# Optimization experiments

Measured on AMD Instinct MI355X. Metric: run time of the kernel, lower is better.

The kernel has to match this reference:

```python
import jax, jax.numpy as jnp
import numpy as np
from jax import lax

B, L = 8192, 64
N_VALUES, EMBED, HIDDEN, OUT = 1000, 64, 128, 128


def setup_inputs() -> dict:
    key = jax.random.key(0)
    ks = jax.random.split(key, 8)
    s = 0.1  # weight scale ~ 1/sqrt(hidden)
    return {
        "x": jax.random.randint(ks[0], (B, L), 0, N_VALUES),
        "embed": jax.random.normal(ks[1], (N_VALUES, EMBED), jnp.float32) * s,
        "W_ih": jax.random.normal(ks[2], (3 * HIDDEN, EMBED), jnp.float32) * s,
        "W_hh": jax.random.normal(ks[3], (3 * HIDDEN, HIDDEN), jnp.float32) * s,
        "b_ih": jax.random.normal(ks[4], (3 * HIDDEN,), jnp.float32) * s,
        "b_hh": jax.random.normal(ks[5], (3 * HIDDEN,), jnp.float32) * s,
        "W_out": jax.random.normal(ks[6], (OUT, HIDDEN), jnp.float32) * s,
        "b_out": jax.random.normal(ks[7], (OUT,), jnp.float32) * s,
    }


def _gru_encode(x, embed, W_ih, W_hh, b_ih, b_hh, W_out, b_out):
    e = embed[x]  # [B, L, E] embedding lookup
    H = W_hh.shape[1]
    # Precompute input-to-gate projections for all timesteps (batched GEMM).
    xg = jnp.einsum('ble,ge->blg', e, W_ih) + b_ih  # [B, L, 3H]

    def step(h, xg_t):
        hg = h @ W_hh.T + b_hh  # [B, 3H]
        xr, xz, xn = jnp.split(xg_t, 3, axis=-1)
        hr, hz, hn = jnp.split(hg, 3, axis=-1)
        r = jax.nn.sigmoid(xr + hr)
        z = jax.nn.sigmoid(xz + hz)
        n = jnp.tanh(xn + r * hn)  # PyTorch GRU: r gates the hidden 'new' term
        h_new = (1.0 - z) * n + z * h
        return h_new, None

    h0 = jnp.zeros((x.shape[0], H), e.dtype)
    h_last, _ = lax.scan(step, h0, jnp.swapaxes(xg, 0, 1))  # scan over time
    return h_last @ W_out.T + b_out  # [B, OUT]


def reference(x, embed, W_ih, W_hh, b_ih, b_hh, W_out, b_out):
    return _gru_encode(x, embed, W_ih, W_hh, b_ih, b_hh, W_out, b_out)
```

## Files before the change

kernel.cpp:

```cpp
#include <hip/hip_runtime.h>


typedef __bf16 bf16x8 __attribute__((ext_vector_type(8)));
typedef float  f32x4  __attribute__((ext_vector_type(4)));
typedef int    int4v  __attribute__((ext_vector_type(4)));
typedef unsigned int uint2v __attribute__((ext_vector_type(2)));

#define NV   1000
#define EMB  64
#define HD   128
#define G3   384
#define SEQ  64
#define BB   16

#define SC_RZ (-1.4426950408889634f)
#define SC_N  ( 2.8853900817779268f)

__device__ __forceinline__ float bflo(unsigned int word) {
    return __builtin_bit_cast(float, word << 16);
}
__device__ __forceinline__ float bfhi(unsigned int word) {
    return __builtin_bit_cast(float, word & 0xffff0000u);
}

__global__ void g_table_kernel(const float* __restrict__ embed,
                               const float* __restrict__ W_ih,
                               const float* __restrict__ b_ih,
                               const float* __restrict__ b_hh,
                               unsigned short* __restrict__ Gpk)
{
    __shared__ float emb[EMB];
    const int v = blockIdx.x;
    const int g = threadIdx.x;
    if (g < EMB) emb[g] = embed[v * EMB + g];
    __syncthreads();
    const float* wr = W_ih + g * EMB;
    float s = b_ih[g] + (g < 2 * HD ? b_hh[g] : 0.f);
    #pragma unroll
    for (int e = 0; e < EMB; e += 4) {
        const float4 w4 = *(const float4*)(wr + e);
        s += w4.x * emb[e] + w4.y * emb[e + 1] + w4.z * emb[e + 2] + w4.w * emb[e + 3];
    }
    const int hid = g & 127, gate = g >> 7;
    s *= (gate < 2) ? SC_RZ : SC_N;
    const int w8 = hid >> 4, c16i = hid & 15;
    Gpk[((v * 8 + w8) * 16 + c16i) * 4 + gate] =
        __builtin_bit_cast(unsigned short, (__bf16)s);
}

#define GRU_STEP(P, T)                                                             \
  {                                                                                \
    __builtin_amdgcn_s_setprio(1);                                                 \
    int4v tk = {0, 0, 0, 0};                                                       \
    if ((T) < SEQ - 1) tk = *(const int4v*)&xl[((T) + 1) * BB + quad * 4];         \
    f32x4 acc[3];                                                                  \
    float xn_[4];                                                                  \
    _Pragma("unroll") for (int j = 0; j < 4; ++j) {                                \
      acc[0][j] = bflo(pf[j][0]);                                \
      acc[1][j] = bfhi(pf[j][0]);                                \
      acc[2][j] = bnw;                                           \
      xn_[j]    = bflo(pf[j][1]);                                \
    }                                                                              \
    _Pragma("unroll") for (int ks = 0; ks < 4; ++ks) {                             \
      const bf16x8 af = *(const bf16x8*)(hbase + (P) * 4096 + aoff[ks]);           \
      _Pragma("unroll") for (int gate = 0; gate < 3; ++gate)                       \
        acc[gate] = __builtin_amdgcn_mfma_f32_16x16x32_bf16(                       \
            af, wf[gate][ks], acc[gate], 0, 0, 0);                                 \
    }                                                                              \
    if ((T) < SEQ - 1) {                                                           \
      _Pragma("unroll") for (int j = 0; j < 4; ++j)                                \
        pf[j] = *(const uint2v*)(gbase + (unsigned)(tk[j] * 1024 + goff));         \
    }                                                                              \
    __builtin_amdgcn_s_setprio(0);                                                 \
    _Pragma("unroll") for (int j = 0; j < 4; ++j) {                                \
      const float Er = __builtin_amdgcn_exp2f(acc[0][j]);                          \
      const float r  = __builtin_amdgcn_rcpf(1.f + Er);                            \
      const float Ez = __builtin_amdgcn_exp2f(acc[1][j]);                          \
      const float a1 = 1.f + Ez;                                                   \
      const float v  = __builtin_fmaf(r, acc[2][j], xn_[j]);                       \
      const float En = __builtin_amdgcn_exp2f(v);                                  \
      const float a2 = 1.f + En;                                                   \
      const float m  = En - 1.f;                                                   \
      const float num = __builtin_fmaf(hreg[j], a2, Ez * m);                       \
      const float rd  = __builtin_amdgcn_rcpf(a1 * a2);                            \
      const float hn  = num * rd;                                                  \
      hreg[j] = hn;                                                                \
      *(unsigned short*)(hbase + (1 - (P)) * 4096 + woff[j]) =                     \
          __builtin_bit_cast(unsigned short, (__bf16)hn);                          \
    }                                                                              \
    asm volatile("s_waitcnt lgkmcnt(0)" ::: "memory");                             \
    __builtin_amdgcn_s_barrier();                                                  \
    __builtin_amdgcn_sched_barrier(0);                                             \
  }

__global__ __launch_bounds__(512, 4) void gru_kernel(
    const int*   __restrict__ x,    const unsigned short* __restrict__ Gpk,
    const float* __restrict__ Whh,  const float* __restrict__ bhh,
    const float* __restrict__ Wout, const float* __restrict__ bout,
    float* __restrict__ out)
{
    __shared__ unsigned short hA[2 * BB * HD];
    __shared__ int xl[SEQ * BB];

    const int tid  = threadIdx.x;
    const int lane = tid & 63;
    const int w    = tid >> 6;
    const int c16  = lane & 15;
    const int quad = lane >> 4;
    const int br0  = blockIdx.x * BB;

    #pragma unroll
    for (int i = 0; i < 2; ++i) {
        const int idx = i * 512 + tid;
        const int r = idx >> 6;
        const int t = idx & 63;
        xl[t * BB + r] = x[(br0 + r) * SEQ + t];
    }
    {
        unsigned int* hA32 = (unsigned int*)hA;
        #pragma unroll
        for (int i = 0; i < 2; ++i)
            hA32[i * 512 + tid] = 0u;
    }

    bf16x8 wf[3][4];
    #pragma unroll
    for (int gate = 0; gate < 3; ++gate)
    #pragma unroll
    for (int ks = 0; ks < 4; ++ks) {
        const float sc = (gate < 2) ? SC_RZ : SC_N;
        const int col = gate * HD + w * 16 + c16;
        const float* p = Whh + col * HD + ks * 32 + quad * 4;
        const float4 a = *(const float4*)p;
        const float4 b = *(const float4*)(p + 16);
        bf16x8 f;
        f[0] = (__bf16)(sc * a.x); f[1] = (__bf16)(sc * a.y);
        f[2] = (__bf16)(sc * a.z); f[3] = (__bf16)(sc * a.w);
        f[4] = (__bf16)(sc * b.x); f[5] = (__bf16)(sc * b.y);
        f[6] = (__bf16)(sc * b.z); f[7] = (__bf16)(sc * b.w);
        wf[gate][ks] = f;
    }

    const float bnw = SC_N * bhh[2 * HD + w * 16 + c16];

    int aoff[4];
    #pragma unroll
    for (int ks = 0; ks < 4; ++ks)
        aoff[ks] = c16 * 256 + ((ks * 64 + quad * 16) ^ ((c16 & 7) << 4));
    int woff[4];
    {
        const int hid  = w * 16 + c16;
        const int sidx = ((hid >> 5) << 5) | (((hid & 15) >> 2) << 3)
                       | (((hid >> 4) & 1) << 2) | (hid & 3);
        #pragma unroll
        for (int j = 0; j < 4; ++j) {
            const int row = quad * 4 + j;
            woff[j] = row * 256 + ((sidx * 2) ^ ((row & 7) << 4));
        }
    }

    char* hbase = (char*)hA;
    const char* gbase = (const char*)Gpk;
    const int goff = w * 128 + c16 * 8;

    float hreg[4] = {0.f, 0.f, 0.f, 0.f};
    const f32x4 z4 = {0.f, 0.f, 0.f, 0.f};

    __syncthreads();

    uint2v pf[4];
    {
        const int4v tk0 = *(const int4v*)&xl[0 * BB + quad * 4];
        #pragma unroll
        for (int j = 0; j < 4; ++j)
            pf[j] = *(const uint2v*)(gbase + (unsigned)(tk0[j] * 1024 + goff));
    }

    for (int tt = 0; tt < SEQ; tt += 2) {
        GRU_STEP(0, tt);
        GRU_STEP(1, tt + 1);
    }

    bf16x8 wo[4];
    #pragma unroll
    for (int ks = 0; ks < 4; ++ks) {
        const int col = w * 16 + c16;
        const float* p = Wout + col * HD + ks * 32 + quad * 4;
        const float4 a = *(const float4*)p;
        const float4 b = *(const float4*)(p + 16);
        bf16x8 f;
        f[0] = (__bf16)a.x; f[1] = (__bf16)a.y; f[2] = (__bf16)a.z; f[3] = (__bf16)a.w;
        f[4] = (__bf16)b.x; f[5] = (__bf16)b.y; f[6] = (__bf16)b.z; f[7] = (__bf16)b.w;
        wo[ks] = f;
    }
    const float bow = bout[w * 16 + c16];

    f32x4 oacc = z4;
    #pragma unroll
    for (int ks = 0; ks < 4; ++ks) {
        const bf16x8 af = *(const bf16x8*)(hbase + aoff[ks]);
        oacc = __builtin_amdgcn_mfma_f32_16x16x32_bf16(af, wo[ks], oacc, 0, 0, 0);
    }
    #pragma unroll
    for (int j = 0; j < 4; ++j) {
        const int row = br0 + quad * 4 + j;
        out[row * HD + w * 16 + c16] = oacc[j] + bow;
    }
}

extern "C" void kernel_launch(void* const* d_in, const int* in_sizes, int n_in,
                              void* d_out, int out_size, void* d_ws, size_t ws_size,
                              hipStream_t stream) {
    const int*   x     = (const int*)  d_in[0];
    const float* embed = (const float*)d_in[1];
    const float* W_ih  = (const float*)d_in[2];
    const float* W_hh  = (const float*)d_in[3];
    const float* b_ih  = (const float*)d_in[4];
    const float* b_hh  = (const float*)d_in[5];
    const float* W_out = (const float*)d_in[6];
    const float* b_out = (const float*)d_in[7];
    float* outp = (float*)d_out;
    unsigned short* Gpk = (unsigned short*)d_ws;

    const int Bsz = in_sizes[0] / SEQ;

    g_table_kernel<<<NV, G3, 0, stream>>>(embed, W_ih, b_ih, b_hh, Gpk);
    gru_kernel<<<Bsz / BB, 512, 0, stream>>>(x, Gpk, W_hh, b_hh, W_out, b_out, outp);
}
```

Measured before the change: 97.97 us.

## Replace per-step block barrier with fine-grained LDS flag polling between waves

Removes the workgroup-wide s_barrier at the end of each GRU timestep. Each wave instead publishes per-wave progress flags in shared memory: one after it finishes reading h and one after it writes its h slice. Before each k-slice MFMA a wave polls only the two producer waves it depends on, and before overwriting the other h buffer it waits for all waves to have finished reading. This lets waves drift relative to each other and overlap work, at the cost of spin-polling with s_sleep and a memory-ordering risk from relying on volatile LDS accesses and waitcnt.

Result: slower. 162.9 us (+66.2%).

```diff
diff --git a/kernel.cpp b/kernel.cpp
--- a/kernel.cpp
+++ b/kernel.cpp
@@ -48,6 +48,23 @@
         __builtin_bit_cast(unsigned short, (__bf16)s);
 }
 
+#define POLL2(i0, i1, T)                                                           \
+  { volatile int* _f = (volatile int*)wfl;                                         \
+    while ((_f[i0] < (T)) | (_f[i1] < (T))) __builtin_amdgcn_s_sleep(1);           \
+    asm volatile("" ::: "memory"); }
+
+#define POLLR(T)                                                                   \
+  { volatile int* _f = (volatile int*)wfl;                                         \
+    for (;;) {                                                                     \
+      int m0 = _f[8]  < (T) ? 1 : 0;  m0 |= _f[9]  < (T);                          \
+      m0 |= _f[10] < (T);  m0 |= _f[11] < (T);                                     \
+      m0 |= _f[12] < (T);  m0 |= _f[13] < (T);                                     \
+      m0 |= _f[14] < (T);  m0 |= _f[15] < (T);                                     \
+      if (!m0) break;                                                              \
+      __builtin_amdgcn_s_sleep(1);                                                 \
+    }                                                                              \
+    asm volatile("" ::: "memory"); }
+
 #define GRU_STEP(P, T)                                                             \
   {                                                                                \
     __builtin_amdgcn_s_setprio(1);                                                 \
@@ -56,22 +73,26 @@
     f32x4 acc[3];                                                                  \
     float xn_[4];                                                                  \
     _Pragma("unroll") for (int j = 0; j < 4; ++j) {                                \
-      acc[0][j] = bflo(pf[j][0]);                                \
-      acc[1][j] = bfhi(pf[j][0]);                                \
-      acc[2][j] = bnw;                                           \
-      xn_[j]    = bflo(pf[j][1]);                                \
+      acc[0][j] = bflo(pf[j][0]);                                         \
+      acc[1][j] = bfhi(pf[j][0]);                                         \
+      acc[2][j] = bnw;                                                    \
+      xn_[j]    = bflo(pf[j][1]);                                         \
     }                                                                              \
     _Pragma("unroll") for (int ks = 0; ks < 4; ++ks) {                             \
+      POLL2(2 * ks, 2 * ks + 1, (T))                                               \
       const bf16x8 af = *(const bf16x8*)(hbase + (P) * 4096 + aoff[ks]);           \
       _Pragma("unroll") for (int gate = 0; gate < 3; ++gate)                       \
         acc[gate] = __builtin_amdgcn_mfma_f32_16x16x32_bf16(                       \
             af, wf[gate][ks], acc[gate], 0, 0, 0);                                 \
     }                                                                              \
+    asm volatile("s_waitcnt lgkmcnt(0)" ::: "memory");                             \
+    if (lane == 0) ((volatile int*)wfl)[8 + w] = (T) + 1;     \
     if ((T) < SEQ - 1) {                                                           \
       _Pragma("unroll") for (int j = 0; j < 4; ++j)                                \
         pf[j] = *(const uint2v*)(gbase + (unsigned)(tk[j] * 1024 + goff));         \
     }                                                                              \
     __builtin_amdgcn_s_setprio(0);                                                 \
+    unsigned short hb[4];                                                          \
     _Pragma("unroll") for (int j = 0; j < 4; ++j) {                                \
       const float Er = __builtin_amdgcn_exp2f(acc[0][j]);                          \
       const float r  = __builtin_amdgcn_rcpf(1.f + Er);                            \
@@ -85,12 +106,13 @@
       const float rd  = __builtin_amdgcn_rcpf(a1 * a2);                            \
       const float hn  = num * rd;                                                  \
       hreg[j] = hn;                                                                \
-      *(unsigned short*)(hbase + (1 - (P)) * 4096 + woff[j]) =                     \
-          __builtin_bit_cast(unsigned short, (__bf16)hn);                          \
-    }                                                                              \
+      hb[j] = __builtin_bit_cast(unsigned short, (__bf16)hn);                      \
+    }                                                                              \
+    POLLR((T))                                      \
+    _Pragma("unroll") for (int j = 0; j < 4; ++j)                                  \
+      *(unsigned short*)(hbase + (1 - (P)) * 4096 + woff[j]) = hb[j];              \
     asm volatile("s_waitcnt lgkmcnt(0)" ::: "memory");                             \
-    __builtin_amdgcn_s_barrier();                                                  \
-    __builtin_amdgcn_sched_barrier(0);                                             \
+    if (lane == 0) ((volatile int*)wfl)[w] = (T) + 1;          \
   }
 
 __global__ __launch_bounds__(512, 4) void gru_kernel(
@@ -101,6 +123,7 @@
 {
     __shared__ unsigned short hA[2 * BB * HD];
     __shared__ int xl[SEQ * BB];
+    __shared__ int wfl[16];
 
     const int tid  = threadIdx.x;
     const int lane = tid & 63;
@@ -122,6 +145,7 @@
         for (int i = 0; i < 2; ++i)
             hA32[i * 512 + tid] = 0u;
     }
+    if (tid < 16) wfl[tid] = 0;
 
     bf16x8 wf[3][4];
     #pragma unroll
@@ -177,8 +201,19 @@
     }
 
     for (int tt = 0; tt < SEQ; tt += 2) {
-        GRU_STEP(0, tt);
-        GRU_STEP(1, tt + 1);
+        GRU_STEP(0, tt)
+        GRU_STEP(1, tt + 1)
+    }
+    {
+        volatile int* _f = (volatile int*)wfl;
+        for (;;) {
+            int bad = _f[0] < SEQ;  bad |= _f[1] < SEQ;  bad |= _f[2] < SEQ;
+            bad |= _f[3] < SEQ;     bad |= _f[4] < SEQ;  bad |= _f[5] < SEQ;
+            bad |= _f[6] < SEQ;     bad |= _f[7] < SEQ;
+            if (!bad) break;
+            __builtin_amdgcn_s_sleep(1);
+        }
+        asm volatile("" ::: "memory");
     }
 
     bf16x8 wo[4];
```
